# Kernel tuning notes

Hardware: AMD Instinct MI355X
Metric: run time of the kernel (lower is better)

The kernel has to match this reference:

```python
import jax, jax.numpy as jnp
import numpy as np

S = 4096      # total packed tokens
B = 8         # number of variable-length segments
E = 1152      # embed_dim (SigLIP2 so400m)
H = 16        # num_heads
D = E // H    # head_dim = 72


def setup_inputs() -> dict:
    key = jax.random.key(0)
    ks = jax.random.split(key, 8)
    w_std = 0.02
    theta = jax.random.uniform(ks[1], (S, D), jnp.float32, 0.0, 2.0 * np.pi)
    return {
        "hidden_states": jax.random.normal(ks[0], (S, E), jnp.float32),
        "cu_seqlens": jnp.arange(B + 1, dtype=jnp.int32) * (S // B),
        "cos": jnp.cos(theta),
        "sin": jnp.sin(theta),
        "Wq": jax.random.normal(ks[2], (E, E), jnp.float32) * w_std,
        "bq": jnp.zeros((E,), jnp.float32),
        "Wk": jax.random.normal(ks[3], (E, E), jnp.float32) * w_std,
        "bk": jnp.zeros((E,), jnp.float32),
        "Wv": jax.random.normal(ks[4], (E, E), jnp.float32) * w_std,
        "bv": jnp.zeros((E,), jnp.float32),
        "Wo": jax.random.normal(ks[5], (E, E), jnp.float32) * w_std,
        "bo": jnp.zeros((E,), jnp.float32),
    }


def _rotate_half(x):
    x1, x2 = jnp.split(x, 2, axis=-1)
    return jnp.concatenate((-x2, x1), axis=-1)


def reference(hidden_states, cu_seqlens, cos, sin, Wq, bq, Wk, bk, Wv, bv, Wo, bo):
    seq_len = hidden_states.shape[0]
    scale = np.float32(D) ** -0.5
    # projections -> [S, H, D]
    q = (hidden_states @ Wq.T + bq).reshape(seq_len, H, D)
    k = (hidden_states @ Wk.T + bk).reshape(seq_len, H, D)
    v = (hidden_states @ Wv.T + bv).reshape(seq_len, H, D)
    # inline RoPE (apply_rotary_pos_emb_vision): cos/sin broadcast over heads
    c = cos[:, None, :]
    s = sin[:, None, :]
    q = q * c + _rotate_half(q) * s
    k = k * c + _rotate_half(k) * s
    # segment id per token from cu_seqlens; block-diagonal attention mask
    seg = jnp.searchsorted(cu_seqlens[1:], jnp.arange(seq_len, dtype=cu_seqlens.dtype), side="right")
    mask = seg[:, None] == seg[None, :]                     # [S, S]
    scores = jnp.einsum("shd,thd->hst", q, k) * scale       # [H, S, S]
    neg = jnp.finfo(scores.dtype).min
    scores = jnp.where(mask[None, :, :], scores, neg)
    probs = jax.nn.softmax(scores, axis=-1)
    attn = jnp.einsum("hst,thd->shd", probs, v).reshape(seq_len, E)
    return attn @ Wo.T + bo
```

## Files before the change

kernel.cpp:

```cpp
#include <hip/hip_runtime.h>
#include <float.h>

#define S_LEN 4096
#define E_DIM 1152
#define NH    16
#define HD    72
#define HD2   36
#define NQKV  3456

typedef __attribute__((ext_vector_type(4))) float f32x4;
typedef __attribute__((ext_vector_type(2))) __fp16 fp16v2;
typedef __attribute__((ext_vector_type(8))) _Float16 f16x8;

__device__ __forceinline__ unsigned short f2h(float f) {
    union { _Float16 h; unsigned short u; } c;
    c.h = (_Float16)f;
    return c.u;
}
__device__ __forceinline__ unsigned pack2h(float a, float b) {
    union { fp16v2 v; unsigned u; } c;
    c.v = __builtin_amdgcn_cvt_pkrtz(a, b);
    return c.u;
}

__device__ __forceinline__ void gload_lds16(const unsigned short* g, unsigned short* l) {
    __builtin_amdgcn_global_load_lds(
        (const __attribute__((address_space(1))) unsigned int*)g,
        (__attribute__((address_space(3))) unsigned int*)l, 16, 0, 0);
}

__global__ __launch_bounds__(256)
void pack_f16(const float* __restrict__ hs, const float* __restrict__ wq,
              const float* __restrict__ wk, const float* __restrict__ wv,
              const float* __restrict__ wo,
              unsigned short* __restrict__ hs_h, unsigned short* __restrict__ wqkv_h,
              unsigned short* __restrict__ wo_h)
{
    const float* src; unsigned short* dst; int n4;
    const int WSZ = E_DIM * E_DIM;
    switch (blockIdx.z) {
        case 0: src = hs; dst = hs_h;             n4 = S_LEN * E_DIM / 4; break;
        case 1: src = wq; dst = wqkv_h;           n4 = WSZ / 4; break;
        case 2: src = wk; dst = wqkv_h + WSZ;     n4 = WSZ / 4; break;
        case 3: src = wv; dst = wqkv_h + 2 * WSZ; n4 = WSZ / 4; break;
        default: src = wo; dst = wo_h;            n4 = WSZ / 4; break;
    }
    for (int i = blockIdx.x * 256 + threadIdx.x; i < n4; i += gridDim.x * 256) {
        f32x4 x = ((const f32x4*)src)[i];
        uint2 hv;
        hv.x = pack2h(x[0], x[1]);
        hv.y = pack2h(x[2], x[3]);
        ((uint2*)dst)[i] = hv;
    }
}

__global__ __launch_bounds__(256, 4)
void gemm_qkv_f16(const unsigned short* __restrict__ Ah, const unsigned short* __restrict__ Wh,
                  const float* __restrict__ bq, const float* __restrict__ bk,
                  const float* __restrict__ bv,
                  float* __restrict__ oq, float* __restrict__ ok, float* __restrict__ ov)
{
    __shared__ unsigned short sA[128 * 64];
    __shared__ unsigned short sB[128 * 64];
    const int tid  = threadIdx.x;
    const int w    = tid >> 6, lane = tid & 63;
    const int quad = lane >> 4, m = lane & 15;
    const int wr   = w & 1,  wc = w >> 1;

    const int bid = blockIdx.x;
    const int lin = (bid & 7) * 108 + (bid >> 3);
    const int n_t = lin >> 5;
    const int m_t = lin & 31;
    const int m0  = m_t * 128;
    const int n0  = n_t * 128;

    const int srow = lane >> 3;
    const int skc  = (lane & 7) ^ srow;

    f32x4 acc[4][4];
    #pragma unroll
    for (int i = 0; i < 4; ++i)
        #pragma unroll
        for (int j = 0; j < 4; ++j) acc[i][j] = (f32x4){0.f, 0.f, 0.f, 0.f};

    const int rm7 = m & 7;

    for (int k0 = 0; k0 < E_DIM; k0 += 64) {
        #pragma unroll
        for (int c = 0; c < 4; ++c) {
            int r = 32 * w + 8 * c + srow;
            gload_lds16(Ah + (size_t)(m0 + r) * E_DIM + k0 + skc * 8, &sA[(32 * w + 8 * c) * 64]);
            gload_lds16(Wh + (size_t)(n0 + r) * E_DIM + k0 + skc * 8, &sB[(32 * w + 8 * c) * 64]);
        }
        __syncthreads();

        #pragma unroll
        for (int k3 = 0; k3 < 2; ++k3) {
            f16x8 ah[4], bh[4];
            #pragma unroll
            for (int t = 0; t < 4; ++t) {
                int pc = ((k3 << 2) + quad) ^ rm7;
                ah[t] = *(const f16x8*)&sA[(64 * wr + 16 * t + m) * 64 + pc * 8];
                bh[t] = *(const f16x8*)&sB[(64 * wc + 16 * t + m) * 64 + pc * 8];
            }
            #pragma unroll
            for (int rt = 0; rt < 4; ++rt)
                #pragma unroll
                for (int ct = 0; ct < 4; ++ct)
                    acc[rt][ct] = __builtin_amdgcn_mfma_f32_16x16x32_f16(ah[rt], bh[ct], acc[rt][ct], 0, 0, 0);
        }
        __syncthreads();
    }

    const int which = n0 / E_DIM;
    const int n0l = n0 - which * E_DIM;
    const float* bp = (which == 0) ? bq : (which == 1) ? bk : bv;
    float* Cp       = (which == 0) ? oq : (which == 1) ? ok : ov;
    #pragma unroll
    for (int ct = 0; ct < 4; ++ct) {
        int col = n0l + 64 * wc + 16 * ct + m;
        float bias = bp[col];
        #pragma unroll
        for (int rt = 0; rt < 4; ++rt)
            #pragma unroll
            for (int reg = 0; reg < 4; ++reg) {
                int row = m0 + 64 * wr + 16 * rt + 4 * quad + reg;
                Cp[(size_t)row * E_DIM + col] = acc[rt][ct][reg] + bias;
            }
    }
}

__global__ __launch_bounds__(256, 4)
void gemm_out_f16(const unsigned short* __restrict__ Ah, const unsigned short* __restrict__ Wh,
                  const float* __restrict__ bo, float* __restrict__ Cp)
{
    __shared__ unsigned short sA[64 * 64];
    __shared__ unsigned short sB[128 * 64];
    const int tid  = threadIdx.x;
    const int w    = tid >> 6, lane = tid & 63;
    const int quad = lane >> 4, m = lane & 15;
    const int m0   = blockIdx.y * 64;
    const int n0   = blockIdx.x * 128;

    const int srow = lane >> 3;
    const int skc  = (lane & 7) ^ srow;

    f32x4 acc[4][2];
    #pragma unroll
    for (int i = 0; i < 4; ++i)
        #pragma unroll
        for (int j = 0; j < 2; ++j) acc[i][j] = (f32x4){0.f, 0.f, 0.f, 0.f};

    const int rm7 = m & 7;

    for (int k0 = 0; k0 < E_DIM; k0 += 64) {
        #pragma unroll
        for (int c = 0; c < 2; ++c) {
            int r = 16 * w + 8 * c + srow;
            gload_lds16(Ah + (size_t)(m0 + r) * E_DIM + k0 + skc * 8, &sA[(16 * w + 8 * c) * 64]);
        }
        #pragma unroll
        for (int c = 0; c < 4; ++c) {
            int r = 32 * w + 8 * c + srow;
            gload_lds16(Wh + (size_t)(n0 + r) * E_DIM + k0 + skc * 8, &sB[(32 * w + 8 * c) * 64]);
        }
        __syncthreads();
        #pragma unroll
        for (int k3 = 0; k3 < 2; ++k3) {
            f16x8 ah[4], bh[2];
            int pc = ((k3 << 2) + quad) ^ rm7;
            #pragma unroll
            for (int t = 0; t < 4; ++t)
                ah[t] = *(const f16x8*)&sA[(16 * t + m) * 64 + pc * 8];
            #pragma unroll
            for (int ct = 0; ct < 2; ++ct)
                bh[ct] = *(const f16x8*)&sB[(32 * w + 16 * ct + m) * 64 + pc * 8];
            #pragma unroll
            for (int rt = 0; rt < 4; ++rt)
                #pragma unroll
                for (int ct = 0; ct < 2; ++ct)
                    acc[rt][ct] = __builtin_amdgcn_mfma_f32_16x16x32_f16(ah[rt], bh[ct], acc[rt][ct], 0, 0, 0);
        }
        __syncthreads();
    }

    #pragma unroll
    for (int ct = 0; ct < 2; ++ct) {
        int col = n0 + 32 * w + 16 * ct + m;
        float bias = bo[col];
        #pragma unroll
        for (int rt = 0; rt < 4; ++rt)
            #pragma unroll
            for (int reg = 0; reg < 4; ++reg) {
                int row = m0 + 16 * rt + 4 * quad + reg;
                Cp[(size_t)row * E_DIM + col] = acc[rt][ct][reg] + bias;
            }
    }
}

__global__ __launch_bounds__(256)
void rope_v_pack(const float* __restrict__ qf, const float* __restrict__ kf,
                 const float* __restrict__ vf,
                 const float* __restrict__ cosb, const float* __restrict__ sinb,
                 unsigned short* __restrict__ qb, unsigned short* __restrict__ kb,
                 unsigned short* __restrict__ vt)
{
    __shared__ unsigned short tile[HD][72];
    const int h  = blockIdx.y;
    const int s0 = blockIdx.x * 64;
    const int z  = blockIdx.z;
    if (z < 2) {
        const float* x = (z == 0) ? qf : kf;
        unsigned short* ob = (z == 0) ? qb : kb;
        for (int task = threadIdx.x; task < 64 * 9; task += 256) {
            int sl = task / 9, c = task % 9;
            int s = s0 + sl;
            int d0 = c << 2;
            const float* xr = x + (size_t)s * E_DIM + h * HD;
            f32x4 a  = *(const f32x4*)(xr + d0);
            f32x4 b  = *(const f32x4*)(xr + d0 + HD2);
            f32x4 c1 = *(const f32x4*)(cosb + (size_t)s * HD + d0);
            f32x4 s1 = *(const f32x4*)(sinb + (size_t)s * HD + d0);
            f32x4 c2 = *(const f32x4*)(cosb + (size_t)s * HD + d0 + HD2);
            f32x4 s2 = *(const f32x4*)(sinb + (size_t)s * HD + d0 + HD2);
            f32x4 r1 = a * c1 - b * s1;
            f32x4 r2 = b * c2 + a * s2;
            unsigned short* orow = ob + ((size_t)h * S_LEN + s) * HD;
            uint2 u1, u2;
            u1.x = pack2h(r1[0], r1[1]); u1.y = pack2h(r1[2], r1[3]);
            u2.x = pack2h(r2[0], r2[1]); u2.y = pack2h(r2[2], r2[3]);
            *(uint2*)(orow + d0)       = u1;
            *(uint2*)(orow + d0 + HD2) = u2;
        }
    } else {
        for (int task = threadIdx.x; task < 64 * 18; task += 256) {
            int r = task / 18, c = task % 18;
            f32x4 x = *(const f32x4*)(vf + (size_t)(s0 + r) * E_DIM + h * HD + (c << 2));
            tile[(c << 2) + 0][r] = f2h(x[0]);
            tile[(c << 2) + 1][r] = f2h(x[1]);
            tile[(c << 2) + 2][r] = f2h(x[2]);
            tile[(c << 2) + 3][r] = f2h(x[3]);
        }
        __syncthreads();
        for (int task = threadIdx.x; task < HD * 8; task += 256) {
            int d = task / 8, cc = task % 8;
            uint4 val = *(const uint4*)&tile[d][cc << 3];
            *(uint4*)(vt + ((size_t)h * HD + d) * S_LEN + s0 + (cc << 3)) = val;
        }
    }
}

__global__ __launch_bounds__(256, 4)
void attn_f16(const unsigned short* __restrict__ qb, const unsigned short* __restrict__ kb,
              const unsigned short* __restrict__ vt, const int* __restrict__ cu,
              int nseg, unsigned short* __restrict__ out)
{
    __shared__ unsigned short ks_s[64][72];
    __shared__ unsigned short vs_s[80][72];

    const int tid  = threadIdx.x;
    const int w    = tid >> 6;
    const int lane = tid & 63;
    const int quad = lane >> 4;
    const int m    = lane & 15;
    const int h    = blockIdx.y;
    const int qb0  = blockIdx.x * 64;
    const float scale = 0.11785113019775793f;

    {
        uint4 zz = make_uint4(0u, 0u, 0u, 0u);
        if (tid < 72) {
            int r = 72 + tid / 9, c = tid % 9;
            *(uint4*)&vs_s[r][c << 3] = zz;
        }
    }

    const int qrow = qb0 + 16 * w + m;
    int st = 0;
    for (int i = 1; i < nseg; ++i) if (cu[i] <= qrow) st = i;
    const int rs = cu[st], re = cu[st + 1];

    int st0 = 0, st1 = 0;
    for (int i = 1; i < nseg; ++i) {
        if (cu[i] <= qb0) st0 = i;
        if (cu[i] <= qb0 + 63) st1 = i;
    }
    const int kstart = cu[st0];
    const int kend   = cu[st1 + 1];

    f16x8 qfr[3];
    {
        const unsigned short* qrp = qb + ((size_t)h * S_LEN + qrow) * HD;
        #pragma unroll
        for (int k3 = 0; k3 < 3; ++k3) {
            bool pad = (k3 == 2) && (quad != 0);
            int off = pad ? 0 : (k3 * 32 + quad * 8);
            f16x8 val = *(const f16x8*)(qrp + off);
            f16x8 z = {0, 0, 0, 0, 0, 0, 0, 0};
            qfr[k3] = pad ? z : val;
        }
    }

    f32x4 acc_o[5];
    #pragma unroll
    for (int i = 0; i < 5; ++i) acc_o[i] = (f32x4){0.f, 0.f, 0.f, 0.f};
    float l_s = 0.f;

    const int srcA = 32 * (quad & 1) + m;
    const bool sel = (quad >> 1) != 0;

    for (int kb_i = kstart; kb_i < kend; kb_i += 64) {
        __syncthreads();
        for (int slot = tid; slot < 64 * 9; slot += 256) {
            int r = slot / 9, c = slot % 9;
            int krow = kb_i + r; if (krow >= kend) krow = kend - 1;
            uint4 val = *(const uint4*)(kb + ((size_t)h * S_LEN + krow) * HD + (c << 3));
            *(uint4*)&ks_s[r][c << 3] = val;
        }
        for (int slot = tid; slot < 72 * 8; slot += 256) {
            int d = slot / 8, c = slot % 8;
            int kk0 = kb_i + (c << 3);
            if (kk0 > S_LEN - 8) kk0 = S_LEN - 8;
            uint4 val = *(const uint4*)(vt + ((size_t)h * HD + d) * S_LEN + kk0);
            *(uint4*)&vs_s[d][c << 3] = val;
        }
        __syncthreads();

        f32x4 sacc[4];
        #pragma unroll
        for (int ct = 0; ct < 4; ++ct) sacc[ct] = (f32x4){0.f, 0.f, 0.f, 0.f};
        #pragma unroll
        for (int ct = 0; ct < 4; ++ct) {
            const unsigned short* krow = &ks_s[16 * ct + m][0];
            #pragma unroll
            for (int k3 = 0; k3 < 3; ++k3) {
                bool pad = (k3 == 2) && (quad != 0);
                int off = pad ? 0 : (k3 * 32 + quad * 8);
                f16x8 kfr = *(const f16x8*)(krow + off);
                f16x8 z = {0, 0, 0, 0, 0, 0, 0, 0};
                kfr = pad ? z : kfr;
                sacc[ct] = __builtin_amdgcn_mfma_f32_16x16x32_f16(kfr, qfr[k3], sacc[ct], 0, 0, 0);
            }
        }

        unsigned pk[4][2];
        #pragma unroll
        for (int ct = 0; ct < 4; ++ct) {
            float p[4];
            #pragma unroll
            for (int reg = 0; reg < 4; ++reg) {
                int key = kb_i + 16 * ct + 4 * quad + reg;
                bool valid = (key >= rs) && (key < re);
                p[reg] = valid ? __expf(sacc[ct][reg] * scale) : 0.f;
                l_s += p[reg];
            }
            pk[ct][0] = pack2h(p[0], p[1]);
            pk[ct][1] = pack2h(p[2], p[3]);
        }

        f16x8 pf[2];
        #pragma unroll
        for (int c = 0; c < 2; ++c) {
            union { unsigned d[4]; f16x8 v; } fb;
            #pragma unroll
            for (int r = 0; r < 2; ++r) {
                int x0 = __shfl((int)pk[2 * c][r],     srcA);
                int x1 = __shfl((int)pk[2 * c + 1][r], srcA);
                fb.d[r] = (unsigned)(sel ? x1 : x0);
                int y0 = __shfl((int)pk[2 * c][r],     srcA + 16);
                int y1 = __shfl((int)pk[2 * c + 1][r], srcA + 16);
                fb.d[2 + r] = (unsigned)(sel ? y1 : y0);
            }
            pf[c] = fb.v;
        }

        #pragma unroll
        for (int ct2 = 0; ct2 < 5; ++ct2) {
            const unsigned short* vrow = &vs_s[16 * ct2 + m][0];
            f16x8 vf0 = *(const f16x8*)(vrow + quad * 8);
            f16x8 vf1 = *(const f16x8*)(vrow + 32 + quad * 8);
            acc_o[ct2] = __builtin_amdgcn_mfma_f32_16x16x32_f16(pf[0], vf0, acc_o[ct2], 0, 0, 0);
            acc_o[ct2] = __builtin_amdgcn_mfma_f32_16x16x32_f16(pf[1], vf1, acc_o[ct2], 0, 0, 0);
        }
    }

    l_s += __shfl_xor(l_s, 16);
    l_s += __shfl_xor(l_s, 32);

    #pragma unroll
    for (int reg = 0; reg < 4; ++reg) {
        float lr = __shfl(l_s, 4 * quad + reg);
        float linv = (lr > 0.f) ? 1.f / lr : 0.f;
        int row = qb0 + 16 * w + 4 * quad + reg;
        unsigned short* orow = out + (size_t)row * E_DIM + h * HD;
        #pragma unroll
        for (int ct2 = 0; ct2 < 5; ++ct2) {
            int col = 16 * ct2 + m;
            if (col < HD) orow[col] = f2h(acc_o[ct2][reg] * linv);
        }
    }
}

extern "C" void kernel_launch(void* const* d_in, const int* in_sizes, int n_in,
                              void* d_out, int out_size, void* d_ws, size_t ws_size,
                              hipStream_t stream)
{
    const float* hs   = (const float*)d_in[0];
    const int*   cu   = (const int*)d_in[1];
    const float* cosb = (const float*)d_in[2];
    const float* sinb = (const float*)d_in[3];
    const float* Wq   = (const float*)d_in[4];
    const float* bq   = (const float*)d_in[5];
    const float* Wk   = (const float*)d_in[6];
    const float* bk   = (const float*)d_in[7];
    const float* Wv   = (const float*)d_in[8];
    const float* bv   = (const float*)d_in[9];
    const float* Wo   = (const float*)d_in[10];
    const float* bo   = (const float*)d_in[11];
    float* outp = (float*)d_out;

    const size_t mat = (size_t)S_LEN * E_DIM;
    float* qf = (float*)d_ws;
    float* kf = qf + mat;
    float* vf = kf + mat;
    unsigned short* hs_h   = (unsigned short*)(vf + mat);
    unsigned short* wqkv_h = hs_h + mat;
    unsigned short* wo_h   = wqkv_h + (size_t)NQKV * E_DIM;
    unsigned short* vtb    = wo_h + (size_t)E_DIM * E_DIM;
    unsigned short* kbb    = vtb + mat;
    unsigned short* qbb    = hs_h;
    unsigned short* attn_h = (unsigned short*)qf;

    const int nseg = in_sizes[1] - 1;

    dim3 gpack(512, 1, 5);
    pack_f16<<<gpack, 256, 0, stream>>>(hs, Wq, Wk, Wv, Wo, hs_h, wqkv_h, wo_h);

    gemm_qkv_f16<<<dim3(864), 256, 0, stream>>>(hs_h, wqkv_h, bq, bk, bv, qf, kf, vf);

    dim3 grv(S_LEN / 64, NH, 3);
    rope_v_pack<<<grv, 256, 0, stream>>>(qf, kf, vf, cosb, sinb, qbb, kbb, vtb);

    dim3 gattn(S_LEN / 64, NH, 1);
    attn_f16<<<gattn, 256, 0, stream>>>(qbb, kbb, vtb, cu, nseg, attn_h);

    dim3 gout(E_DIM / 128, S_LEN / 64, 1);
    gemm_out_f16<<<gout, 256, 0, stream>>>(attn_h, wo_h, bo, outp);
}
```

Baseline: 228.1 us.

## Fuse Q RoPE into attention and process two query tiles per block

Q RoPE and the fp16 conversion move from the pack kernel into the attention kernel, which now reads fp32 Q directly and stages the rotated values in shared memory. Each attention block now covers 128 query rows as two 64-row sets that share every K/V tile loaded into shared memory. This halves K/V tile traffic and removes a Q round-trip through global memory. In exchange, register pressure rises (occupancy hint lowered to 3), the grid has half as many blocks (512), and the key range per block can span more segments.

```diff
diff --git a/kernel.cpp b/kernel.cpp
--- a/kernel.cpp
+++ b/kernel.cpp
@@ -199,24 +199,19 @@
 }
 
 __global__ __launch_bounds__(256)
-void rope_v_pack(const float* __restrict__ qf, const float* __restrict__ kf,
-                 const float* __restrict__ vf,
+void rope_v_pack(const float* __restrict__ kf, const float* __restrict__ vf,
                  const float* __restrict__ cosb, const float* __restrict__ sinb,
-                 unsigned short* __restrict__ qb, unsigned short* __restrict__ kb,
-                 unsigned short* __restrict__ vt)
+                 unsigned short* __restrict__ kb, unsigned short* __restrict__ vt)
 {
     __shared__ unsigned short tile[HD][72];
     const int h  = blockIdx.y;
     const int s0 = blockIdx.x * 64;
-    const int z  = blockIdx.z;
-    if (z < 2) {
-        const float* x = (z == 0) ? qf : kf;
-        unsigned short* ob = (z == 0) ? qb : kb;
+    if (blockIdx.z == 0) {
         for (int task = threadIdx.x; task < 64 * 9; task += 256) {
             int sl = task / 9, c = task % 9;
             int s = s0 + sl;
             int d0 = c << 2;
-            const float* xr = x + (size_t)s * E_DIM + h * HD;
+            const float* xr = kf + (size_t)s * E_DIM + h * HD;
             f32x4 a  = *(const f32x4*)(xr + d0);
             f32x4 b  = *(const f32x4*)(xr + d0 + HD2);
             f32x4 c1 = *(const f32x4*)(cosb + (size_t)s * HD + d0);
@@ -225,7 +220,7 @@
             f32x4 s2 = *(const f32x4*)(sinb + (size_t)s * HD + d0 + HD2);
             f32x4 r1 = a * c1 - b * s1;
             f32x4 r2 = b * c2 + a * s2;
-            unsigned short* orow = ob + ((size_t)h * S_LEN + s) * HD;
+            unsigned short* orow = kb + ((size_t)h * S_LEN + s) * HD;
             uint2 u1, u2;
             u1.x = pack2h(r1[0], r1[1]); u1.y = pack2h(r1[2], r1[3]);
             u2.x = pack2h(r2[0], r2[1]); u2.y = pack2h(r2[2], r2[3]);
@@ -250,10 +245,11 @@
     }
 }
 
-__global__ __launch_bounds__(256, 4)
-void attn_f16(const unsigned short* __restrict__ qb, const unsigned short* __restrict__ kb,
-              const unsigned short* __restrict__ vt, const int* __restrict__ cu,
-              int nseg, unsigned short* __restrict__ out)
+__global__ __launch_bounds__(256, 3)
+void attn_f16(const float* __restrict__ qf, const unsigned short* __restrict__ kb,
+              const unsigned short* __restrict__ vt,
+              const float* __restrict__ cosb, const float* __restrict__ sinb,
+              const int* __restrict__ cu, int nseg, unsigned short* __restrict__ out)
 {
     __shared__ unsigned short ks_s[64][72];
     __shared__ unsigned short vs_s[80][72];
@@ -264,7 +260,7 @@
     const int quad = lane >> 4;
     const int m    = lane & 15;
     const int h    = blockIdx.y;
-    const int qb0  = blockIdx.x * 64;
+    const int qb0  = blockIdx.x * 128;
     const float scale = 0.11785113019775793f;
 
     {
@@ -275,36 +271,64 @@
         }
     }
 
-    const int qrow = qb0 + 16 * w + m;
-    int st = 0;
-    for (int i = 1; i < nseg; ++i) if (cu[i] <= qrow) st = i;
-    const int rs = cu[st], re = cu[st + 1];
-
+    int rs[2], re[2];
+    #pragma unroll
+    for (int set = 0; set < 2; ++set) {
+        int qrow = qb0 + 64 * set + 16 * w + m;
+        int st = 0;
+        for (int i = 1; i < nseg; ++i) if (cu[i] <= qrow) st = i;
+        rs[set] = cu[st];
+        re[set] = cu[st + 1];
+    }
     int st0 = 0, st1 = 0;
     for (int i = 1; i < nseg; ++i) {
         if (cu[i] <= qb0) st0 = i;
-        if (cu[i] <= qb0 + 63) st1 = i;
+        if (cu[i] <= qb0 + 127) st1 = i;
     }
     const int kstart = cu[st0];
     const int kend   = cu[st1 + 1];
 
-    f16x8 qfr[3];
-    {
-        const unsigned short* qrp = qb + ((size_t)h * S_LEN + qrow) * HD;
+    f16x8 qfr[2][3];
+    #pragma unroll
+    for (int set = 0; set < 2; ++set) {
+        __syncthreads();
+        for (int task = tid; task < 64 * 9; task += 256) {
+            int row = task / 9, c = task % 9;
+            int s = qb0 + 64 * set + row;
+            int d0 = c << 2;
+            const float* xr = qf + (size_t)s * E_DIM + h * HD;
+            f32x4 a  = *(const f32x4*)(xr + d0);
+            f32x4 b  = *(const f32x4*)(xr + d0 + HD2);
+            f32x4 c1 = *(const f32x4*)(cosb + (size_t)s * HD + d0);
+            f32x4 s1 = *(const f32x4*)(sinb + (size_t)s * HD + d0);
+            f32x4 c2 = *(const f32x4*)(cosb + (size_t)s * HD + d0 + HD2);
+            f32x4 s2 = *(const f32x4*)(sinb + (size_t)s * HD + d0 + HD2);
+            f32x4 r1 = a * c1 - b * s1;
+            f32x4 r2 = b * c2 + a * s2;
+            uint2 u1, u2;
+            u1.x = pack2h(r1[0], r1[1]); u1.y = pack2h(r1[2], r1[3]);
+            u2.x = pack2h(r2[0], r2[1]); u2.y = pack2h(r2[2], r2[3]);
+            *(uint2*)&ks_s[row][d0]       = u1;
+            *(uint2*)&ks_s[row][d0 + HD2] = u2;
+        }
+        __syncthreads();
+        const unsigned short* qrp = &ks_s[16 * w + m][0];
         #pragma unroll
         for (int k3 = 0; k3 < 3; ++k3) {
             bool pad = (k3 == 2) && (quad != 0);
             int off = pad ? 0 : (k3 * 32 + quad * 8);
             f16x8 val = *(const f16x8*)(qrp + off);
             f16x8 z = {0, 0, 0, 0, 0, 0, 0, 0};
-            qfr[k3] = pad ? z : val;
-        }
-    }
-
-    f32x4 acc_o[5];
-    #pragma unroll
-    for (int i = 0; i < 5; ++i) acc_o[i] = (f32x4){0.f, 0.f, 0.f, 0.f};
-    float l_s = 0.f;
+            qfr[set][k3] = pad ? z : val;
+        }
+    }
+
+    f32x4 acc_o[2][5];
+    #pragma unroll
+    for (int set = 0; set < 2; ++set)
+        #pragma unroll
+        for (int i = 0; i < 5; ++i) acc_o[set][i] = (f32x4){0.f, 0.f, 0.f, 0.f};
+    float l_s[2] = {0.f, 0.f};
 
     const int srcA = 32 * (quad & 1) + m;
     const bool sel = (quad >> 1) != 0;
@@ -326,77 +350,83 @@
         }
         __syncthreads();
 
-        f32x4 sacc[4];
-        #pragma unroll
-        for (int ct = 0; ct < 4; ++ct) sacc[ct] = (f32x4){0.f, 0.f, 0.f, 0.f};
-        #pragma unroll
-        for (int ct = 0; ct < 4; ++ct) {
-            const unsigned short* krow = &ks_s[16 * ct + m][0];
-            #pragma unroll
-            for (int k3 = 0; k3 < 3; ++k3) {
-                bool pad = (k3 == 2) && (quad != 0);
-                int off = pad ? 0 : (k3 * 32 + quad * 8);
-                f16x8 kfr = *(const f16x8*)(krow + off);
-                f16x8 z = {0, 0, 0, 0, 0, 0, 0, 0};
-                kfr = pad ? z : kfr;
-                sacc[ct] = __builtin_amdgcn_mfma_f32_16x16x32_f16(kfr, qfr[k3], sacc[ct], 0, 0, 0);
-            }
-        }
-
-        unsigned pk[4][2];
-        #pragma unroll
-        for (int ct = 0; ct < 4; ++ct) {
-            float p[4];
-            #pragma unroll
-            for (int reg = 0; reg < 4; ++reg) {
-                int key = kb_i + 16 * ct + 4 * quad + reg;
-                bool valid = (key >= rs) && (key < re);
-                p[reg] = valid ? __expf(sacc[ct][reg] * scale) : 0.f;
-                l_s += p[reg];
-            }
-            pk[ct][0] = pack2h(p[0], p[1]);
-            pk[ct][1] = pack2h(p[2], p[3]);
-        }
-
-        f16x8 pf[2];
-        #pragma unroll
-        for (int c = 0; c < 2; ++c) {
-            union { unsigned d[4]; f16x8 v; } fb;
-            #pragma unroll
-            for (int r = 0; r < 2; ++r) {
-                int x0 = __shfl((int)pk[2 * c][r],     srcA);
-                int x1 = __shfl((int)pk[2 * c + 1][r], srcA);
-                fb.d[r] = (unsigned)(sel ? x1 : x0);
-                int y0 = __shfl((int)pk[2 * c][r],     srcA + 16);
-                int y1 = __shfl((int)pk[2 * c + 1][r], srcA + 16);
-                fb.d[2 + r] = (unsigned)(sel ? y1 : y0);
-            }
-            pf[c] = fb.v;
-        }
-
-        #pragma unroll
-        for (int ct2 = 0; ct2 < 5; ++ct2) {
-            const unsigned short* vrow = &vs_s[16 * ct2 + m][0];
-            f16x8 vf0 = *(const f16x8*)(vrow + quad * 8);
-            f16x8 vf1 = *(const f16x8*)(vrow + 32 + quad * 8);
-            acc_o[ct2] = __builtin_amdgcn_mfma_f32_16x16x32_f16(pf[0], vf0, acc_o[ct2], 0, 0, 0);
-            acc_o[ct2] = __builtin_amdgcn_mfma_f32_16x16x32_f16(pf[1], vf1, acc_o[ct2], 0, 0, 0);
-        }
-    }
-
-    l_s += __shfl_xor(l_s, 16);
-    l_s += __shfl_xor(l_s, 32);
-
-    #pragma unroll
-    for (int reg = 0; reg < 4; ++reg) {
-        float lr = __shfl(l_s, 4 * quad + reg);
-        float linv = (lr > 0.f) ? 1.f / lr : 0.f;
-        int row = qb0 + 16 * w + 4 * quad + reg;
-        unsigned short* orow = out + (size_t)row * E_DIM + h * HD;
-        #pragma unroll
-        for (int ct2 = 0; ct2 < 5; ++ct2) {
-            int col = 16 * ct2 + m;
-            if (col < HD) orow[col] = f2h(acc_o[ct2][reg] * linv);
+        #pragma unroll
+        for (int set = 0; set < 2; ++set) {
+            f32x4 sacc[4];
+            #pragma unroll
+            for (int ct = 0; ct < 4; ++ct) sacc[ct] = (f32x4){0.f, 0.f, 0.f, 0.f};
+            #pragma unroll
+            for (int ct = 0; ct < 4; ++ct) {
+                const unsigned short* krow = &ks_s[16 * ct + m][0];
+                #pragma unroll
+                for (int k3 = 0; k3 < 3; ++k3) {
+                    bool pad = (k3 == 2) && (quad != 0);
+                    int off = pad ? 0 : (k3 * 32 + quad * 8);
+                    f16x8 kfr = *(const f16x8*)(krow + off);
+                    f16x8 z = {0, 0, 0, 0, 0, 0, 0, 0};
+                    kfr = pad ? z : kfr;
+                    sacc[ct] = __builtin_amdgcn_mfma_f32_16x16x32_f16(kfr, qfr[set][k3], sacc[ct], 0, 0, 0);
+                }
+            }
+
+            unsigned pk[4][2];
+            #pragma unroll
+            for (int ct = 0; ct < 4; ++ct) {
+                float p[4];
+                #pragma unroll
+                for (int reg = 0; reg < 4; ++reg) {
+                    int key = kb_i + 16 * ct + 4 * quad + reg;
+                    bool valid = (key >= rs[set]) && (key < re[set]);
+                    p[reg] = valid ? __expf(sacc[ct][reg] * scale) : 0.f;
+                    l_s[set] += p[reg];
+                }
+                pk[ct][0] = pack2h(p[0], p[1]);
+                pk[ct][1] = pack2h(p[2], p[3]);
+            }
+
+            f16x8 pf[2];
+            #pragma unroll
+            for (int c = 0; c < 2; ++c) {
+                union { unsigned d[4]; f16x8 v; } fb;
+                #pragma unroll
+                for (int r = 0; r < 2; ++r) {
+                    int x0 = __shfl((int)pk[2 * c][r],     srcA);
+                    int x1 = __shfl((int)pk[2 * c + 1][r], srcA);
+                    fb.d[r] = (unsigned)(sel ? x1 : x0);
+                    int y0 = __shfl((int)pk[2 * c][r],     srcA + 16);
+                    int y1 = __shfl((int)pk[2 * c + 1][r], srcA + 16);
+                    fb.d[2 + r] = (unsigned)(sel ? y1 : y0);
+                }
+                pf[c] = fb.v;
+            }
+
+            #pragma unroll
+            for (int ct2 = 0; ct2 < 5; ++ct2) {
+                const unsigned short* vrow = &vs_s[16 * ct2 + m][0];
+                f16x8 vf0 = *(const f16x8*)(vrow + quad * 8);
+                f16x8 vf1 = *(const f16x8*)(vrow + 32 + quad * 8);
+                acc_o[set][ct2] = __builtin_amdgcn_mfma_f32_16x16x32_f16(pf[0], vf0, acc_o[set][ct2], 0, 0, 0);
+                acc_o[set][ct2] = __builtin_amdgcn_mfma_f32_16x16x32_f16(pf[1], vf1, acc_o[set][ct2], 0, 0, 0);
+            }
+        }
+    }
+
+    #pragma unroll
+    for (int set = 0; set < 2; ++set) {
+        float l = l_s[set];
+        l += __shfl_xor(l, 16);
+        l += __shfl_xor(l, 32);
+        #pragma unroll
+        for (int reg = 0; reg < 4; ++reg) {
+            float lr = __shfl(l, 4 * quad + reg);
+            float linv = (lr > 0.f) ? 1.f / lr : 0.f;
+            int row = qb0 + 64 * set + 16 * w + 4 * quad + reg;
+            unsigned short* orow = out + (size_t)row * E_DIM + h * HD;
+            #pragma unroll
+            for (int ct2 = 0; ct2 < 5; ++ct2) {
+                int col = 16 * ct2 + m;
+                if (col < HD) orow[col] = f2h(acc_o[set][ct2][reg] * linv);
+            }
         }
     }
 }
@@ -428,8 +458,7 @@
     unsigned short* wo_h   = wqkv_h + (size_t)NQKV * E_DIM;
     unsigned short* vtb    = wo_h + (size_t)E_DIM * E_DIM;
     unsigned short* kbb    = vtb + mat;
-    unsigned short* qbb    = hs_h;
-    unsigned short* attn_h = (unsigned short*)qf;
+    unsigned short* attn_h = hs_h;
 
     const int nseg = in_sizes[1] - 1;
 
@@ -438,11 +467,11 @@
 
     gemm_qkv_f16<<<dim3(864), 256, 0, stream>>>(hs_h, wqkv_h, bq, bk, bv, qf, kf, vf);
 
-    dim3 grv(S_LEN / 64, NH, 3);
-    rope_v_pack<<<grv, 256, 0, stream>>>(qf, kf, vf, cosb, sinb, qbb, kbb, vtb);
-
-    dim3 gattn(S_LEN / 64, NH, 1);
-    attn_f16<<<gattn, 256, 0, stream>>>(qbb, kbb, vtb, cu, nseg, attn_h);
+    dim3 grv(S_LEN / 64, NH, 2);
+    rope_v_pack<<<grv, 256, 0, stream>>>(kf, vf, cosb, sinb, kbb, vtb);
+
+    dim3 gattn(S_LEN / 128, NH, 1);
+    attn_f16<<<gattn, 256, 0, stream>>>(qf, kbb, vtb, cosb, sinb, cu, nseg, attn_h);
 
     dim3 gout(E_DIM / 128, S_LEN / 64, 1);
     gemm_out_f16<<<gout, 256, 0, stream>>>(attn_h, wo_h, bo, outp);
```

New measurement: 247.0 us. 1.08x slower.
